# Performance work log

Measured on AMD Instinct MI355X. Metric: run time of the kernel, lower is better.

Reference implementation:

```python
import jax, jax.numpy as jnp
import numpy as np

N_NODES = 100000
N_EDGES = 1600000
D_IN = 128
D_H = 128
D_OUT = 64


def _glorot(key, shape):
    fan_in, fan_out = shape[0], shape[1]
    lim = np.sqrt(6.0 / (fan_in + fan_out)).astype(np.float32)
    return jax.random.uniform(key, shape, jnp.float32, -lim, lim)


def setup_inputs() -> dict:
    key = jax.random.key(0)
    ks = jax.random.split(key, 12)
    x = jax.random.normal(ks[0], (N_NODES, D_IN), jnp.float32)
    edge_index = jax.random.randint(ks[1], (2, N_EDGES), 0, N_NODES, jnp.int64)
    return {
        'x': x,
        'edge_index': edge_index,
        'Wl0': _glorot(ks[2], (D_IN, D_H)),  'bl0': jnp.zeros((D_H,), jnp.float32), 'Wr0': _glorot(ks[3], (D_IN, D_H)),
        'Wl1': _glorot(ks[4], (D_H, D_H)),   'bl1': jnp.zeros((D_H,), jnp.float32), 'Wr1': _glorot(ks[5], (D_H, D_H)),
        'Wl2': _glorot(ks[6], (D_H, D_H)),   'bl2': jnp.zeros((D_H,), jnp.float32), 'Wr2': _glorot(ks[7], (D_H, D_H)),
        'W':   _glorot(ks[8], (D_H, D_OUT)), 'b':   jnp.zeros((D_OUT,), jnp.float32),
    }


def _sage_conv(x, src, dst, inv_deg, Wl, bl, Wr):
    # mean aggregation of neighbor features at dst, then lin_l(agg) + lin_r(x)
    agg = jax.ops.segment_sum(x[src], dst, num_segments=N_NODES)  # [N, d]
    mean = agg * inv_deg  # [N, d]
    return mean @ Wl + bl + x @ Wr


def reference(x, edge_index, Wl0, bl0, Wr0, Wl1, bl1, Wr1, Wl2, bl2, Wr2, W, b):
    src, dst = edge_index[0], edge_index[1]
    deg = jax.ops.segment_sum(jnp.ones((N_EDGES,), jnp.float32), dst, num_segments=N_NODES)
    inv_deg = (1.0 / jnp.maximum(deg, 1.0))[:, None]  # [N, 1]
    h = jax.nn.relu(_sage_conv(x, src, dst, inv_deg, Wl0, bl0, Wr0))
    h = jax.nn.relu(_sage_conv(h, src, dst, inv_deg, Wl1, bl1, Wr1))
    h = jax.nn.relu(_sage_conv(h, src, dst, inv_deg, Wl2, bl2, Wr2))
    return h @ W + b
```

## Files before the change

### kernel.cpp

```cpp
#include <hip/hip_runtime.h>
#include <cstddef>

#define N_NODES 100000
#define N_EDGES 1600000
#define D 128
#define NB 782
#define CAP 3072
#define NBLK 1000
#define CHUNK 1600
#define OROW 784
#define WTOT (6 * 16384 + 8192)

typedef unsigned int u32;
typedef unsigned long long u64;
typedef float f32x4 __attribute__((ext_vector_type(4)));
typedef _Float16 f16x8 __attribute__((ext_vector_type(8)));

__device__ inline f16x8 mk16(u64 a, u64 b) {
  union { u64 q[2]; f16x8 v; } u;
  u.q[0] = a; u.q[1] = b;
  return u.v;
}

__device__ inline void acc8(float* a, uint2 d, float c) {
  a[0] += (float)(d.x & 0xFFu) * c;
  a[1] += (float)((d.x >> 8) & 0xFFu) * c;
  a[2] += (float)((d.x >> 16) & 0xFFu) * c;
  a[3] += (float)(d.x >> 24) * c;
  a[4] += (float)(d.y & 0xFFu) * c;
  a[5] += (float)((d.y >> 8) & 0xFFu) * c;
  a[6] += (float)((d.y >> 16) & 0xFFu) * c;
  a[7] += (float)(d.y >> 24) * c;
}

__device__ inline u64 dq4(u32 w, float c, float n) {
  float f0 = fmaf((float)(w & 0xFFu), c, n);
  float f1 = fmaf((float)((w >> 8) & 0xFFu), c, n);
  float f2 = fmaf((float)((w >> 16) & 0xFFu), c, n);
  float f3 = fmaf((float)(w >> 24), c, n);
  auto lo = __builtin_amdgcn_cvt_pkrtz(f0, f1);
  auto hi = __builtin_amdgcn_cvt_pkrtz(f2, f3);
  return (u64)__builtin_bit_cast(u32, lo) | ((u64)__builtin_bit_cast(u32, hi) << 32);
}


__global__ __launch_bounds__(256) void k_prep(
    const float* __restrict__ x,
    unsigned char* __restrict__ x8, float* __restrict__ sx,
    const float* __restrict__ w0, const float* __restrict__ w1, const float* __restrict__ w2,
    const float* __restrict__ w3, const float* __restrict__ w4, const float* __restrict__ w5,
    const float* __restrict__ w6, unsigned short* __restrict__ wt16) {
  int bid = blockIdx.x;
  int tid = threadIdx.x;
  if (bid < 6250) {
    int row = bid * 16 + (tid >> 4);
    int sub = tid & 15;
    const float* xr = x + (size_t)row * D + sub * 8;
    float4 v0 = *(const float4*)xr;
    float4 v1 = *(const float4*)(xr + 4);
    float vs[8] = {v0.x, v0.y, v0.z, v0.w, v1.x, v1.y, v1.z, v1.w};
    float m = 0.f;
#pragma unroll
    for (int j = 0; j < 8; j++) m = fmaxf(m, fabsf(vs[j]));
#pragma unroll
    for (int off = 1; off < 16; off <<= 1) m = fmaxf(m, __shfl_xor(m, off));
    m = fmaxf(m, 1e-8f);
    float inv = 127.0f / m;
    u64 pk = 0;
#pragma unroll
    for (int j = 0; j < 8; j++) {
      int qi = (int)rintf(vs[j] * inv) + 128;
      pk |= (u64)(u32)(qi & 255) << (8 * j);
    }
    *(u64*)(x8 + (size_t)row * D + sub * 8) = pk;
    if (sub == 0) sx[row] = m / 127.0f;
    return;
  }
  int i = (bid - 6250) * 256 + tid;
  if (i >= WTOT) return;
  float v;
  if (i < 6 * 16384) {
    int m = i >> 14;
    int j = i & 16383;
    int c = j >> 7, k = j & 127;
    const float* w = (m == 0) ? w0 : (m == 1) ? w1 : (m == 2) ? w2
                   : (m == 3) ? w3 : (m == 4) ? w4 : w5;
    v = w[k * 128 + c];
  } else {
    int j = i - 6 * 16384;
    int c = j >> 7, k = j & 127;
    v = w6[k * 64 + c];
  }
  _Float16 h = (_Float16)v;
  wt16[i] = __builtin_bit_cast(unsigned short, h);
}


__global__ __launch_bounds__(256) void k_scatter(const int* __restrict__ src,
                                                 const int* __restrict__ dst,
                                                 u32* __restrict__ binned,
                                                 u32* __restrict__ offs) {
  __shared__ int cnt[NB];
  __shared__ int lbase[NB + 1];
  __shared__ int wsum[256];
  __shared__ u32 stage[CHUNK];
  const int tid = threadIdx.x;
  for (int i = tid; i < NB; i += 256) cnt[i] = 0;
  __syncthreads();
  const int e0 = blockIdx.x * CHUNK;
  for (int e = e0 + tid; e < e0 + CHUNK; e += 256)
    atomicAdd(&cnt[dst[e] >> 7], 1);
  __syncthreads();
  int c[4], s = 0;
#pragma unroll
  for (int j = 0; j < 4; j++) {
    int i = tid * 4 + j;
    c[j] = (i < NB) ? cnt[i] : 0;
    s += c[j];
  }
  wsum[tid] = s;
  __syncthreads();
  for (int off = 1; off < 256; off <<= 1) {
    int t = (tid >= off) ? wsum[tid - off] : 0;
    __syncthreads();
    wsum[tid] += t;
    __syncthreads();
  }
  int run = wsum[tid] - s;
#pragma unroll
  for (int j = 0; j < 4; j++) {
    int i = tid * 4 + j;
    if (i < NB) { lbase[i] = run; run += c[j]; }
  }
  if (tid == 0) lbase[NB] = CHUNK;
  __syncthreads();
  for (int i = tid; i < NB; i += 256) cnt[i] = 0;
  __syncthreads();
  for (int e = e0 + tid; e < e0 + CHUNK; e += 256) {
    int d = dst[e];
    int bkt = d >> 7;
    int l = atomicAdd(&cnt[bkt], 1);
    stage[lbase[bkt] + l] = ((u32)(d & 127) << 17) | (u32)src[e];
  }
  u32* orow = offs + (size_t)blockIdx.x * OROW;
  for (int i = tid; i <= NB; i += 256) orow[i] = (u32)lbase[i];
  __syncthreads();
  u32* bseg = binned + (size_t)blockIdx.x * CHUNK;
  for (int i = tid; i < CHUNK / 4; i += 256)
    *(uint4*)(bseg + i * 4) = *(const uint4*)(stage + i * 4);
}


__global__ __launch_bounds__(256) void k_build(const u32* __restrict__ binned,
                                               const u32* __restrict__ offs,
                                               int* __restrict__ row_start,
                                               int* __restrict__ row_end,
                                               float* __restrict__ inv_deg,
                                               int* __restrict__ csr_src) {
  __shared__ u32 stage[CAP];
  __shared__ int deg[128], sc[128], cur[128];
  __shared__ int fill;
  const int b = blockIdx.x;
  const int tid = threadIdx.x;
  if (tid == 0) fill = 0;
  if (tid < 128) deg[tid] = 0;
  __syncthreads();
  for (int k = tid; k < NBLK; k += 256) {
    const u32* orow = offs + (size_t)k * OROW;
    int o0 = (int)orow[b], o1 = (int)orow[b + 1];
    int n = o1 - o0;
    if (n > 0) {
      int p = atomicAdd(&fill, n);
      const u32* q = binned + (size_t)k * CHUNK + o0;
      for (int j = 0; j < n; ++j) stage[p + j] = q[j];
    }
  }
  __syncthreads();
  const int total = fill;
  for (int e = tid; e < total; e += 256)
    atomicAdd(&deg[stage[e] >> 17], 1);
  __syncthreads();
  int dv = (tid < 128) ? deg[tid] : 0;
  if (tid < 128) sc[tid] = dv;
  __syncthreads();
  for (int off = 1; off < 128; off <<= 1) {
    int t = (tid >= off && tid < 128) ? sc[tid - off] : 0;
    __syncthreads();
    if (tid < 128) sc[tid] += t;
    __syncthreads();
  }
  const int cbase = b * CAP;
  if (tid < 128) {
    int excl = sc[tid] - dv;
    cur[tid] = excl;
    int node = (b << 7) + tid;
    if (node < N_NODES) {
      row_start[node] = cbase + excl;
      row_end[node] = cbase + excl + dv;
      inv_deg[node] = 1.0f / fmaxf((float)dv, 1.0f);
    }
  }
  __syncthreads();
  for (int e = tid; e < total; e += 256) {
    u32 w = stage[e];
    int dl = w >> 17;
    int pos = cbase + atomicAdd(&cur[dl], 1);
    csr_src[pos] = (int)(w & 0x1FFFFu);
  }
}


template <bool BIN, bool BOUT>
__global__ __launch_bounds__(256) void k_agg(const unsigned char* __restrict__ q8,
                                             const float* __restrict__ qs,
                                             const int* __restrict__ row_start,
                                             const int* __restrict__ row_end,
                                             const float* __restrict__ inv_deg,
                                             const int* __restrict__ csr_src,
                                             unsigned char* __restrict__ out8,
                                             float* __restrict__ sout) {
  int node = blockIdx.x * 16 + (threadIdx.x >> 4);
  if (node >= N_NODES) return;
  int sub = threadIdx.x & 15;
  int p0 = row_start[node], p1 = row_end[node];
  float a[8];
#pragma unroll
  for (int j = 0; j < 8; j++) a[j] = 0.f;
  float ssum = 0.f;
  int p = p0;
  for (; p + 8 <= p1; p += 8) {
    int s0 = csr_src[p], s1 = csr_src[p + 1], s2 = csr_src[p + 2], s3 = csr_src[p + 3];
    int s4 = csr_src[p + 4], s5 = csr_src[p + 5], s6 = csr_src[p + 6], s7 = csr_src[p + 7];
    uint2 d0 = *(const uint2*)(q8 + (size_t)s0 * D + sub * 8);
    uint2 d1 = *(const uint2*)(q8 + (size_t)s1 * D + sub * 8);
    uint2 d2 = *(const uint2*)(q8 + (size_t)s2 * D + sub * 8);
    uint2 d3 = *(const uint2*)(q8 + (size_t)s3 * D + sub * 8);
    uint2 d4 = *(const uint2*)(q8 + (size_t)s4 * D + sub * 8);
    uint2 d5 = *(const uint2*)(q8 + (size_t)s5 * D + sub * 8);
    uint2 d6 = *(const uint2*)(q8 + (size_t)s6 * D + sub * 8);
    uint2 d7 = *(const uint2*)(q8 + (size_t)s7 * D + sub * 8);
    float c0 = qs[s0], c1 = qs[s1], c2 = qs[s2], c3 = qs[s3];
    float c4 = qs[s4], c5 = qs[s5], c6 = qs[s6], c7 = qs[s7];
    acc8(a, d0, c0); acc8(a, d1, c1); acc8(a, d2, c2); acc8(a, d3, c3);
    acc8(a, d4, c4); acc8(a, d5, c5); acc8(a, d6, c6); acc8(a, d7, c7);
    if (BIN) ssum += ((c0 + c1) + (c2 + c3)) + ((c4 + c5) + (c6 + c7));
  }
  for (; p + 2 <= p1; p += 2) {
    int s0 = csr_src[p], s1 = csr_src[p + 1];
    uint2 d0 = *(const uint2*)(q8 + (size_t)s0 * D + sub * 8);
    uint2 d1 = *(const uint2*)(q8 + (size_t)s1 * D + sub * 8);
    float c0 = qs[s0], c1 = qs[s1];
    acc8(a, d0, c0); acc8(a, d1, c1);
    if (BIN) ssum += c0 + c1;
  }
  if (p < p1) {
    int s0 = csr_src[p];
    uint2 d0 = *(const uint2*)(q8 + (size_t)s0 * D + sub * 8);
    float c0 = qs[s0];
    acc8(a, d0, c0);
    if (BIN) ssum += c0;
  }
  float scl = inv_deg[node];
  float v[8];
#pragma unroll
  for (int j = 0; j < 8; j++) {
    float t = a[j];
    if (BIN) t -= 128.0f * ssum;
    v[j] = t * scl;
  }
  float m = 0.f;
#pragma unroll
  for (int j = 0; j < 8; j++) m = fmaxf(m, BOUT ? fabsf(v[j]) : v[j]);
#pragma unroll
  for (int off = 1; off < 16; off <<= 1) m = fmaxf(m, __shfl_xor(m, off));
  m = fmaxf(m, 1e-8f);
  u64 pk = 0;
  if (BOUT) {
    float inv = 127.0f / m;
#pragma unroll
    for (int j = 0; j < 8; j++) {
      int qi = (int)rintf(v[j] * inv) + 128;
      pk |= (u64)(u32)(qi & 255) << (8 * j);
    }
  } else {
    float inv = 255.0f / m;
#pragma unroll
    for (int j = 0; j < 8; j++) {
      u32 qi = (u32)(v[j] * inv + 0.5f);
      pk |= (u64)(qi & 255) << (8 * j);
    }
  }
  *(u64*)(out8 + (size_t)node * D + sub * 8) = pk;
  if (sub == 0) sout[node] = m / (BOUT ? 127.0f : 255.0f);
}


template <bool B0, bool B1>
__global__ __launch_bounds__(256) void k_gemm(
    const unsigned char* __restrict__ in0, const float* __restrict__ s0,
    const unsigned char* __restrict__ in1, const float* __restrict__ s1,
    const unsigned short* __restrict__ wt, const float* __restrict__ bias,
    unsigned char* __restrict__ h8out, float* __restrict__ shout) {
  __shared__ u64 sI[128][9];
  __shared__ u64 sW[128][9];
  __shared__ u32 rmaxb[128];
  __shared__ unsigned char h8t[128 * 144];

  const int tid = threadIdx.x;
  const int row0 = blockIdx.x * 128;
  const int lane = tid & 63;
  const int w = tid >> 6;
  const int wr = w >> 1, wc = w & 1;
  const int lrow = lane & 15, kb = lane >> 4;
  const int sr = tid >> 2, sq = tid & 3;

  f32x4 acc[4][4];
#pragma unroll
  for (int i = 0; i < 4; i++)
#pragma unroll
    for (int j = 0; j < 4; j++) acc[i][j] = (f32x4){0.f, 0.f, 0.f, 0.f};

  uint2 rd[2]; float rc[2];
  u64 rW[2][2];

  auto loadA = [&](int ch) {
    const unsigned char* inP = (ch >= 4) ? in1 : in0;
    const float* sP = (ch >= 4) ? s1 : s0;
    const int kc = (ch & 3) * 32;
#pragma unroll
    for (int it = 0; it < 2; ++it) {
      int g = row0 + sr + it * 64;
      uint2 d = make_uint2(0, 0);
      float c = 0.f;
      if (g < N_NODES) {
        d = *(const uint2*)(inP + (size_t)g * D + kc + sq * 8);
        c = sP[g];
      }
      rd[it] = d; rc[it] = c;
    }
  };
  auto loadW = [&](int ch) {
    const int s = ch >> 2;
    const int kc = (ch & 3) * 32;
    const unsigned short* wP = wt + (size_t)s * 16384;
#pragma unroll
    for (int it = 0; it < 2; ++it) {
      int c = sr + it * 64;
      const u64* pp = (const u64*)(wP + (size_t)c * D + kc + sq * 8);
      rW[it][0] = pp[0]; rW[it][1] = pp[1];
    }
  };

  loadA(0); loadW(0);
#pragma unroll
  for (int ch = 0; ch < 8; ++ch) {
    const bool biased = (ch < 4) ? B0 : B1;
    __syncthreads();
#pragma unroll
    for (int it = 0; it < 2; ++it) {
      int r = sr + it * 64;
      float c = rc[it];
      float n = biased ? -128.0f * c : 0.0f;
      sI[r][sq * 2] = dq4(rd[it].x, c, n);
      sI[r][sq * 2 + 1] = dq4(rd[it].y, c, n);
      sW[r][sq * 2] = rW[it][0]; sW[r][sq * 2 + 1] = rW[it][1];
    }
    __syncthreads();
    if (ch < 7) { loadA(ch + 1); loadW(ch + 1); }

    f16x8 fA[4], fB[4];
#pragma unroll
    for (int rt = 0; rt < 4; ++rt) {
      int rr = wr * 64 + rt * 16 + lrow;
      fA[rt] = mk16(sI[rr][kb * 2], sI[rr][kb * 2 + 1]);
    }
#pragma unroll
    for (int ct = 0; ct < 4; ++ct) {
      int cc = wc * 64 + ct * 16 + lrow;
      fB[ct] = mk16(sW[cc][kb * 2], sW[cc][kb * 2 + 1]);
    }
#pragma unroll
    for (int ct = 0; ct < 4; ++ct)
#pragma unroll
      for (int rt = 0; rt < 4; ++rt)
        acc[rt][ct] = __builtin_amdgcn_mfma_f32_16x16x32_f16(fA[rt], fB[ct], acc[rt][ct], 0, 0, 0);
  }

  if (tid < 128) rmaxb[tid] = 0;
  float bv[4];
#pragma unroll
  for (int ct = 0; ct < 4; ++ct) bv[ct] = bias[wc * 64 + ct * 16 + lrow];
#pragma unroll
  for (int ct = 0; ct < 4; ++ct)
#pragma unroll
    for (int rt = 0; rt < 4; ++rt)
#pragma unroll
      for (int r = 0; r < 4; ++r)
        acc[rt][ct][r] = fmaxf(acc[rt][ct][r] + bv[ct], 0.f);
  __syncthreads();
#pragma unroll
  for (int rt = 0; rt < 4; ++rt) {
#pragma unroll
    for (int r = 0; r < 4; ++r) {
      float m = fmaxf(fmaxf(acc[rt][0][r], acc[rt][1][r]),
                      fmaxf(acc[rt][2][r], acc[rt][3][r]));
      m = fmaxf(m, __shfl_xor(m, 1));
      m = fmaxf(m, __shfl_xor(m, 2));
      m = fmaxf(m, __shfl_xor(m, 4));
      m = fmaxf(m, __shfl_xor(m, 8));
      if (lrow == 0)
        atomicMax(&rmaxb[wr * 64 + rt * 16 + kb * 4 + r], __float_as_uint(m));
    }
  }
  __syncthreads();
#pragma unroll
  for (int rt = 0; rt < 4; ++rt) {
#pragma unroll
    for (int r = 0; r < 4; ++r) {
      int row = wr * 64 + rt * 16 + kb * 4 + r;
      float rm = fmaxf(__uint_as_float(rmaxb[row]), 1e-8f);
      float inv = 255.0f / rm;
#pragma unroll
      for (int ct = 0; ct < 4; ++ct) {
        u32 q = (u32)(acc[rt][ct][r] * inv + 0.5f);
        h8t[row * 144 + wc * 64 + ct * 16 + lrow] = (unsigned char)q;
      }
    }
  }
  __syncthreads();
  for (int idx = tid; idx < 128 * 8; idx += 256) {
    int row = idx >> 3, qq = idx & 7;
    int g = row0 + row;
    if (g < N_NODES)
      *(uint4*)(h8out + (size_t)g * D + qq * 16) =
          *(const uint4*)(h8t + row * 144 + qq * 16);
  }
  if (tid < 128 && row0 + tid < N_NODES)
    shout[row0 + tid] = fmaxf(__uint_as_float(rmaxb[tid]), 1e-8f) / 255.0f;
}


template <bool B0, bool B1>
__global__ __launch_bounds__(256) void k_gemm2(
    const unsigned char* __restrict__ in0, const float* __restrict__ s0,
    const unsigned char* __restrict__ in1, const float* __restrict__ s1,
    const unsigned short* __restrict__ wt, const float* __restrict__ bias,
    const unsigned short* __restrict__ w2, const float* __restrict__ b2,
    float* __restrict__ outp) {
  __shared__ __align__(16) char smem[128 * 33 * 8 + 2 * 128 * 9 * 8];
  u64 (*sH3)[33] = (u64(*)[33])smem;
  u64 (*sI)[9] = (u64(*)[9])(smem + 128 * 33 * 8);
  u64 (*sW)[9] = (u64(*)[9])(smem + 128 * 33 * 8 + 128 * 9 * 8);
  u64 (*sW2)[33] = (u64(*)[33])(smem + 128 * 33 * 8);

  const int tid = threadIdx.x;
  const int row0 = blockIdx.x * 128;
  const int lane = tid & 63;
  const int w = tid >> 6;
  const int wr = w >> 1, wc = w & 1;
  const int lrow = lane & 15, kb = lane >> 4;
  const int sr = tid >> 2, sq = tid & 3;

  f32x4 acc[4][4];
#pragma unroll
  for (int i = 0; i < 4; i++)
#pragma unroll
    for (int j = 0; j < 4; j++) acc[i][j] = (f32x4){0.f, 0.f, 0.f, 0.f};

  uint2 rd[2]; float rc[2];
  u64 rW[2][2];

  auto loadA = [&](int ch) {
    const unsigned char* inP = (ch >= 4) ? in1 : in0;
    const float* sP = (ch >= 4) ? s1 : s0;
    const int kc = (ch & 3) * 32;
#pragma unroll
    for (int it = 0; it < 2; ++it) {
      int g = row0 + sr + it * 64;
      uint2 d = make_uint2(0, 0);
      float c = 0.f;
      if (g < N_NODES) {
        d = *(const uint2*)(inP + (size_t)g * D + kc + sq * 8);
        c = sP[g];
      }
      rd[it] = d; rc[it] = c;
    }
  };
  auto loadW = [&](int ch) {
    const int s = ch >> 2;
    const int kc = (ch & 3) * 32;
    const unsigned short* wP = wt + (size_t)s * 16384;
#pragma unroll
    for (int it = 0; it < 2; ++it) {
      int c = sr + it * 64;
      const u64* pp = (const u64*)(wP + (size_t)c * D + kc + sq * 8);
      rW[it][0] = pp[0]; rW[it][1] = pp[1];
    }
  };

  loadA(0); loadW(0);
#pragma unroll
  for (int ch = 0; ch < 8; ++ch) {
    const bool biased = (ch < 4) ? B0 : B1;
    __syncthreads();
#pragma unroll
    for (int it = 0; it < 2; ++it) {
      int r = sr + it * 64;
      float c = rc[it];
      float n = biased ? -128.0f * c : 0.0f;
      sI[r][sq * 2] = dq4(rd[it].x, c, n);
      sI[r][sq * 2 + 1] = dq4(rd[it].y, c, n);
      sW[r][sq * 2] = rW[it][0]; sW[r][sq * 2 + 1] = rW[it][1];
    }
    __syncthreads();
    if (ch < 7) { loadA(ch + 1); loadW(ch + 1); }

    f16x8 fA[4], fB[4];
#pragma unroll
    for (int rt = 0; rt < 4; ++rt) {
      int rr = wr * 64 + rt * 16 + lrow;
      fA[rt] = mk16(sI[rr][kb * 2], sI[rr][kb * 2 + 1]);
    }
#pragma unroll
    for (int ct = 0; ct < 4; ++ct) {
      int cc = wc * 64 + ct * 16 + lrow;
      fB[ct] = mk16(sW[cc][kb * 2], sW[cc][kb * 2 + 1]);
    }
#pragma unroll
    for (int ct = 0; ct < 4; ++ct)
#pragma unroll
      for (int rt = 0; rt < 4; ++rt)
        acc[rt][ct] = __builtin_amdgcn_mfma_f32_16x16x32_f16(fA[rt], fB[ct], acc[rt][ct], 0, 0, 0);
  }

#pragma unroll
  for (int ct = 0; ct < 4; ++ct) {
    int col = wc * 64 + ct * 16 + lrow;
    float bv = bias[col];
#pragma unroll
    for (int rt = 0; rt < 4; ++rt) {
      int rbase = wr * 64 + rt * 16 + kb * 4;
#pragma unroll
      for (int r = 0; r < 4; ++r) {
        float v = fmaxf(acc[rt][ct][r] + bv, 0.f);
        _Float16 hv = (_Float16)v;
        ((unsigned short*)(&sH3[rbase + r][0]))[col] = __builtin_bit_cast(unsigned short, hv);
      }
    }
  }
  __syncthreads();
  for (int idx = tid; idx < 64 * 32; idx += 256) {
    int c = idx >> 5, j = idx & 31;
    sW2[c][j] = ((const u64*)(w2 + (size_t)c * D))[j];
  }
  __syncthreads();

  f32x4 acc2[4][2];
#pragma unroll
  for (int i = 0; i < 4; i++)
#pragma unroll
    for (int j = 0; j < 2; j++) acc2[i][j] = (f32x4){0.f, 0.f, 0.f, 0.f};

#pragma unroll
  for (int kc2 = 0; kc2 < 4; ++kc2) {
    f16x8 fA[4], fB[2];
#pragma unroll
    for (int rt = 0; rt < 4; ++rt) {
      int rr = wr * 64 + rt * 16 + lrow;
      fA[rt] = mk16(sH3[rr][kc2 * 8 + kb * 2], sH3[rr][kc2 * 8 + kb * 2 + 1]);
    }
#pragma unroll
    for (int ct = 0; ct < 2; ++ct) {
      int cc = wc * 32 + ct * 16 + lrow;
      fB[ct] = mk16(sW2[cc][kc2 * 8 + kb * 2], sW2[cc][kc2 * 8 + kb * 2 + 1]);
    }
#pragma unroll
    for (int ct = 0; ct < 2; ++ct)
#pragma unroll
      for (int rt = 0; rt < 4; ++rt)
        acc2[rt][ct] =
            __builtin_amdgcn_mfma_f32_16x16x32_f16(fA[rt], fB[ct], acc2[rt][ct], 0, 0, 0);
  }

#pragma unroll
  for (int ct = 0; ct < 2; ++ct) {
    int col = wc * 32 + ct * 16 + lrow;
    float bv = b2[col];
#pragma unroll
    for (int rt = 0; rt < 4; ++rt) {
#pragma unroll
      for (int r = 0; r < 4; ++r) {
        int g = row0 + wr * 64 + rt * 16 + kb * 4 + r;
        if (g < N_NODES) outp[(size_t)g * 64 + col] = acc2[rt][ct][r] + bv;
      }
    }
  }
}


extern "C" void kernel_launch(void* const* d_in, const int* in_sizes, int n_in,
                              void* d_out, int out_size, void* d_ws, size_t ws_size,
                              hipStream_t stream) {
  const float* x = (const float*)d_in[0];
  const int* edge = (const int*)d_in[1];
  const int* src = edge;
  const int* dst = edge + N_EDGES;
  const float* Wl0 = (const float*)d_in[2];
  const float* bl0 = (const float*)d_in[3];
  const float* Wr0 = (const float*)d_in[4];
  const float* Wl1 = (const float*)d_in[5];
  const float* bl1 = (const float*)d_in[6];
  const float* Wr1 = (const float*)d_in[7];
  const float* Wl2 = (const float*)d_in[8];
  const float* bl2 = (const float*)d_in[9];
  const float* Wr2 = (const float*)d_in[10];
  const float* W = (const float*)d_in[11];
  const float* b = (const float*)d_in[12];
  float* out = (float*)d_out;
  (void)ws_size; (void)n_in; (void)in_sizes; (void)out_size;

  char* ws = (char*)d_ws;
  float* sx = (float*)(ws);
  float* sh = (float*)(ws + (512ll << 10));
  float* sa = (float*)(ws + (1ll << 20));
  int* row_start = (int*)(ws + (2ll << 20));
  int* row_end = (int*)(ws + (3ll << 20));
  float* inv_deg = (float*)(ws + (4ll << 20));
  int* csr_src = (int*)(ws + (5ll << 20));
  u32* offs = (u32*)(ws + (15ll << 20));
  unsigned short* wt16 = (unsigned short*)(ws + (19ll << 20));
  unsigned char* agg8 = (unsigned char*)(ws + (20ll << 20));
  unsigned char* x8 = (unsigned char*)(ws + (33ll << 20));
  unsigned char* h8 = (unsigned char*)(ws + (46ll << 20));
  u32* binned = (u32*)(ws + (59ll << 20));

  k_prep<<<6250 + (WTOT + 255) / 256, 256, 0, stream>>>(
      x, x8, sx, Wl0, Wr0, Wl1, Wr1, Wl2, Wr2, W, wt16);
  k_scatter<<<NBLK, 256, 0, stream>>>(src, dst, binned, offs);
  k_build<<<NB, 256, 0, stream>>>(binned, offs, row_start, row_end, inv_deg, csr_src);

  const int agg_grid = (N_NODES + 15) / 16;
  const int gemm_grid = (N_NODES + 127) / 128;

  k_agg<true, true><<<agg_grid, 256, 0, stream>>>(
      x8, sx, row_start, row_end, inv_deg, csr_src, agg8, sa);
  k_gemm<true, true><<<gemm_grid, 256, 0, stream>>>(
      agg8, sa, x8, sx, wt16 + 0, bl0, h8, sh);
  k_agg<false, false><<<agg_grid, 256, 0, stream>>>(
      h8, sh, row_start, row_end, inv_deg, csr_src, agg8, sa);
  k_gemm<false, false><<<gemm_grid, 256, 0, stream>>>(
      agg8, sa, h8, sh, wt16 + 32768, bl1, h8, sh);
  k_agg<false, false><<<agg_grid, 256, 0, stream>>>(
      h8, sh, row_start, row_end, inv_deg, csr_src, agg8, sa);
  k_gemm2<false, false><<<gemm_grid, 256, 0, stream>>>(
      agg8, sa, h8, sh, wt16 + 65536, bl2, wt16 + 98304, b, out);
}
```

Baseline: 250.6 us.

## Merge edge scatter into prep kernel and widen aggregation gathers to 16 bytes

The edge-binning scatter is folded into the prep kernel as an extra range of blocks, removing one kernel launch and letting binning run alongside x quantization and weight conversion. The aggregation kernel now uses 8 lanes per node, each gathering 16 bytes per neighbor instead of 8. Neighbor indices and scales are loaded cooperatively once per group of eight edges and broadcast with shuffles. This cuts redundant index and scale loads and the number of gather instructions, at the cost of more registers per thread and a larger shared-memory footprint for all prep blocks.

Measured after the change: 263.8 us. +5.2%, slower.

```diff
diff --git a/kernel.cpp b/kernel.cpp
--- a/kernel.cpp
+++ b/kernel.cpp
@@ -10,6 +10,8 @@
 #define CHUNK 1600
 #define OROW 784
 #define WTOT (6 * 16384 + 8192)
+#define XBLK 6250
+#define WBLK ((WTOT + 255) / 256)
 
 typedef unsigned int u32;
 typedef unsigned long long u64;
@@ -22,15 +24,15 @@
   return u.v;
 }
 
-__device__ inline void acc8(float* a, uint2 d, float c) {
-  a[0] += (float)(d.x & 0xFFu) * c;
-  a[1] += (float)((d.x >> 8) & 0xFFu) * c;
-  a[2] += (float)((d.x >> 16) & 0xFFu) * c;
-  a[3] += (float)(d.x >> 24) * c;
-  a[4] += (float)(d.y & 0xFFu) * c;
-  a[5] += (float)((d.y >> 8) & 0xFFu) * c;
-  a[6] += (float)((d.y >> 16) & 0xFFu) * c;
-  a[7] += (float)(d.y >> 24) * c;
+__device__ inline void acc8(float* a, u32 dx, u32 dy, float c) {
+  a[0] += (float)(dx & 0xFFu) * c;
+  a[1] += (float)((dx >> 8) & 0xFFu) * c;
+  a[2] += (float)((dx >> 16) & 0xFFu) * c;
+  a[3] += (float)(dx >> 24) * c;
+  a[4] += (float)(dy & 0xFFu) * c;
+  a[5] += (float)((dy >> 8) & 0xFFu) * c;
+  a[6] += (float)((dy >> 16) & 0xFFu) * c;
+  a[7] += (float)(dy >> 24) * c;
 }
 
 __device__ inline u64 dq4(u32 w, float c, float n) {
@@ -49,11 +51,64 @@
     unsigned char* __restrict__ x8, float* __restrict__ sx,
     const float* __restrict__ w0, const float* __restrict__ w1, const float* __restrict__ w2,
     const float* __restrict__ w3, const float* __restrict__ w4, const float* __restrict__ w5,
-    const float* __restrict__ w6, unsigned short* __restrict__ wt16) {
-  int bid = blockIdx.x;
-  int tid = threadIdx.x;
-  if (bid < 6250) {
-    int row = bid * 16 + (tid >> 4);
+    const float* __restrict__ w6, unsigned short* __restrict__ wt16,
+    const int* __restrict__ src, const int* __restrict__ dst,
+    u32* __restrict__ binned, u32* __restrict__ offs) {
+  __shared__ int cnt[NB];
+  __shared__ int lbase[NB + 1];
+  __shared__ int wsum[256];
+  __shared__ u32 stage[CHUNK];
+  const int bid = blockIdx.x;
+  const int tid = threadIdx.x;
+
+  if (bid < NBLK) {
+    for (int i = tid; i < NB; i += 256) cnt[i] = 0;
+    __syncthreads();
+    const int e0 = bid * CHUNK;
+    for (int e = e0 + tid; e < e0 + CHUNK; e += 256)
+      atomicAdd(&cnt[dst[e] >> 7], 1);
+    __syncthreads();
+    int c[4], s = 0;
+#pragma unroll
+    for (int j = 0; j < 4; j++) {
+      int i = tid * 4 + j;
+      c[j] = (i < NB) ? cnt[i] : 0;
+      s += c[j];
+    }
+    wsum[tid] = s;
+    __syncthreads();
+    for (int off = 1; off < 256; off <<= 1) {
+      int t = (tid >= off) ? wsum[tid - off] : 0;
+      __syncthreads();
+      wsum[tid] += t;
+      __syncthreads();
+    }
+    int run = wsum[tid] - s;
+#pragma unroll
+    for (int j = 0; j < 4; j++) {
+      int i = tid * 4 + j;
+      if (i < NB) { lbase[i] = run; run += c[j]; }
+    }
+    if (tid == 0) lbase[NB] = CHUNK;
+    __syncthreads();
+    for (int i = tid; i < NB; i += 256) cnt[i] = 0;
+    __syncthreads();
+    for (int e = e0 + tid; e < e0 + CHUNK; e += 256) {
+      int d = dst[e];
+      int bkt = d >> 7;
+      int l = atomicAdd(&cnt[bkt], 1);
+      stage[lbase[bkt] + l] = ((u32)(d & 127) << 17) | (u32)src[e];
+    }
+    u32* orow = offs + (size_t)bid * OROW;
+    for (int i = tid; i <= NB; i += 256) orow[i] = (u32)lbase[i];
+    __syncthreads();
+    u32* bseg = binned + (size_t)bid * CHUNK;
+    for (int i = tid; i < CHUNK / 4; i += 256)
+      *(uint4*)(bseg + i * 4) = *(const uint4*)(stage + i * 4);
+    return;
+  }
+  if (bid < NBLK + XBLK) {
+    int row = (bid - NBLK) * 16 + (tid >> 4);
     int sub = tid & 15;
     const float* xr = x + (size_t)row * D + sub * 8;
     float4 v0 = *(const float4*)xr;
@@ -76,7 +131,7 @@
     if (sub == 0) sx[row] = m / 127.0f;
     return;
   }
-  int i = (bid - 6250) * 256 + tid;
+  int i = (bid - NBLK - XBLK) * 256 + tid;
   if (i >= WTOT) return;
   float v;
   if (i < 6 * 16384) {
@@ -96,61 +151,6 @@
 }
 
 
-__global__ __launch_bounds__(256) void k_scatter(const int* __restrict__ src,
-                                                 const int* __restrict__ dst,
-                                                 u32* __restrict__ binned,
-                                                 u32* __restrict__ offs) {
-  __shared__ int cnt[NB];
-  __shared__ int lbase[NB + 1];
-  __shared__ int wsum[256];
-  __shared__ u32 stage[CHUNK];
-  const int tid = threadIdx.x;
-  for (int i = tid; i < NB; i += 256) cnt[i] = 0;
-  __syncthreads();
-  const int e0 = blockIdx.x * CHUNK;
-  for (int e = e0 + tid; e < e0 + CHUNK; e += 256)
-    atomicAdd(&cnt[dst[e] >> 7], 1);
-  __syncthreads();
-  int c[4], s = 0;
-#pragma unroll
-  for (int j = 0; j < 4; j++) {
-    int i = tid * 4 + j;
-    c[j] = (i < NB) ? cnt[i] : 0;
-    s += c[j];
-  }
-  wsum[tid] = s;
-  __syncthreads();
-  for (int off = 1; off < 256; off <<= 1) {
-    int t = (tid >= off) ? wsum[tid - off] : 0;
-    __syncthreads();
-    wsum[tid] += t;
-    __syncthreads();
-  }
-  int run = wsum[tid] - s;
-#pragma unroll
-  for (int j = 0; j < 4; j++) {
-    int i = tid * 4 + j;
-    if (i < NB) { lbase[i] = run; run += c[j]; }
-  }
-  if (tid == 0) lbase[NB] = CHUNK;
-  __syncthreads();
-  for (int i = tid; i < NB; i += 256) cnt[i] = 0;
-  __syncthreads();
-  for (int e = e0 + tid; e < e0 + CHUNK; e += 256) {
-    int d = dst[e];
-    int bkt = d >> 7;
-    int l = atomicAdd(&cnt[bkt], 1);
-    stage[lbase[bkt] + l] = ((u32)(d & 127) << 17) | (u32)src[e];
-  }
-  u32* orow = offs + (size_t)blockIdx.x * OROW;
-  for (int i = tid; i <= NB; i += 256) orow[i] = (u32)lbase[i];
-  __syncthreads();
-  u32* bseg = binned + (size_t)blockIdx.x * CHUNK;
-  for (int i = tid; i < CHUNK / 4; i += 256)
-    *(uint4*)(bseg + i * 4) = *(const uint4*)(stage + i * 4);
-}
-
-
 __global__ __launch_bounds__(256) void k_build(const u32* __restrict__ binned,
                                                const u32* __restrict__ offs,
                                                int* __restrict__ row_start,
@@ -219,78 +219,73 @@
                                              const int* __restrict__ csr_src,
                                              unsigned char* __restrict__ out8,
                                              float* __restrict__ sout) {
-  int node = blockIdx.x * 16 + (threadIdx.x >> 4);
+  int node = blockIdx.x * 32 + (threadIdx.x >> 3);
   if (node >= N_NODES) return;
-  int sub = threadIdx.x & 15;
+  int sub = threadIdx.x & 7;
   int p0 = row_start[node], p1 = row_end[node];
-  float a[8];
-#pragma unroll
-  for (int j = 0; j < 8; j++) a[j] = 0.f;
+  float a[16];
+#pragma unroll
+  for (int j = 0; j < 16; j++) a[j] = 0.f;
   float ssum = 0.f;
   int p = p0;
   for (; p + 8 <= p1; p += 8) {
-    int s0 = csr_src[p], s1 = csr_src[p + 1], s2 = csr_src[p + 2], s3 = csr_src[p + 3];
-    int s4 = csr_src[p + 4], s5 = csr_src[p + 5], s6 = csr_src[p + 6], s7 = csr_src[p + 7];
-    uint2 d0 = *(const uint2*)(q8 + (size_t)s0 * D + sub * 8);
-    uint2 d1 = *(const uint2*)(q8 + (size_t)s1 * D + sub * 8);
-    uint2 d2 = *(const uint2*)(q8 + (size_t)s2 * D + sub * 8);
-    uint2 d3 = *(const uint2*)(q8 + (size_t)s3 * D + sub * 8);
-    uint2 d4 = *(const uint2*)(q8 + (size_t)s4 * D + sub * 8);
-    uint2 d5 = *(const uint2*)(q8 + (size_t)s5 * D + sub * 8);
-    uint2 d6 = *(const uint2*)(q8 + (size_t)s6 * D + sub * 8);
-    uint2 d7 = *(const uint2*)(q8 + (size_t)s7 * D + sub * 8);
-    float c0 = qs[s0], c1 = qs[s1], c2 = qs[s2], c3 = qs[s3];
-    float c4 = qs[s4], c5 = qs[s5], c6 = qs[s6], c7 = qs[s7];
-    acc8(a, d0, c0); acc8(a, d1, c1); acc8(a, d2, c2); acc8(a, d3, c3);
-    acc8(a, d4, c4); acc8(a, d5, c5); acc8(a, d6, c6); acc8(a, d7, c7);
-    if (BIN) ssum += ((c0 + c1) + (c2 + c3)) + ((c4 + c5) + (c6 + c7));
-  }
-  for (; p + 2 <= p1; p += 2) {
-    int s0 = csr_src[p], s1 = csr_src[p + 1];
-    uint2 d0 = *(const uint2*)(q8 + (size_t)s0 * D + sub * 8);
-    uint2 d1 = *(const uint2*)(q8 + (size_t)s1 * D + sub * 8);
-    float c0 = qs[s0], c1 = qs[s1];
-    acc8(a, d0, c0); acc8(a, d1, c1);
-    if (BIN) ssum += c0 + c1;
-  }
-  if (p < p1) {
-    int s0 = csr_src[p];
-    uint2 d0 = *(const uint2*)(q8 + (size_t)s0 * D + sub * 8);
-    float c0 = qs[s0];
-    acc8(a, d0, c0);
-    if (BIN) ssum += c0;
+    int myidx = csr_src[p + sub];
+    float myc = qs[myidx];
+#pragma unroll
+    for (int j = 0; j < 8; j++) {
+      int s = __shfl(myidx, j, 8);
+      float c = __shfl(myc, j, 8);
+      uint4 d = *(const uint4*)(q8 + (size_t)s * D + sub * 16);
+      acc8(a, d.x, d.y, c);
+      acc8(a + 8, d.z, d.w, c);
+      if (BIN) ssum += c;
+    }
+  }
+  for (; p < p1; ++p) {
+    int s = csr_src[p];
+    float c = qs[s];
+    uint4 d = *(const uint4*)(q8 + (size_t)s * D + sub * 16);
+    acc8(a, d.x, d.y, c);
+    acc8(a + 8, d.z, d.w, c);
+    if (BIN) ssum += c;
   }
   float scl = inv_deg[node];
-  float v[8];
-#pragma unroll
-  for (int j = 0; j < 8; j++) {
+  float v[16];
+#pragma unroll
+  for (int j = 0; j < 16; j++) {
     float t = a[j];
     if (BIN) t -= 128.0f * ssum;
     v[j] = t * scl;
   }
   float m = 0.f;
 #pragma unroll
-  for (int j = 0; j < 8; j++) m = fmaxf(m, BOUT ? fabsf(v[j]) : v[j]);
-#pragma unroll
-  for (int off = 1; off < 16; off <<= 1) m = fmaxf(m, __shfl_xor(m, off));
+  for (int j = 0; j < 16; j++) m = fmaxf(m, BOUT ? fabsf(v[j]) : v[j]);
+#pragma unroll
+  for (int off = 1; off < 8; off <<= 1) m = fmaxf(m, __shfl_xor(m, off));
   m = fmaxf(m, 1e-8f);
-  u64 pk = 0;
+  u64 pk0 = 0, pk1 = 0;
   if (BOUT) {
     float inv = 127.0f / m;
 #pragma unroll
     for (int j = 0; j < 8; j++) {
-      int qi = (int)rintf(v[j] * inv) + 128;
-      pk |= (u64)(u32)(qi & 255) << (8 * j);
+      int q0 = (int)rintf(v[j] * inv) + 128;
+      int q1 = (int)rintf(v[j + 8] * inv) + 128;
+      pk0 |= (u64)(u32)(q0 & 255) << (8 * j);
+      pk1 |= (u64)(u32)(q1 & 255) << (8 * j);
     }
   } else {
     float inv = 255.0f / m;
 #pragma unroll
     for (int j = 0; j < 8; j++) {
-      u32 qi = (u32)(v[j] * inv + 0.5f);
-      pk |= (u64)(qi & 255) << (8 * j);
-    }
-  }
-  *(u64*)(out8 + (size_t)node * D + sub * 8) = pk;
+      u32 q0 = (u32)(v[j] * inv + 0.5f);
+      u32 q1 = (u32)(v[j + 8] * inv + 0.5f);
+      pk0 |= (u64)(q0 & 255) << (8 * j);
+      pk1 |= (u64)(q1 & 255) << (8 * j);
+    }
+  }
+  union { u64 q[2]; uint4 u; } st;
+  st.q[0] = pk0; st.q[1] = pk1;
+  *(uint4*)(out8 + (size_t)node * D + sub * 16) = st.u;
   if (sub == 0) sout[node] = m / (BOUT ? 127.0f : 255.0f);
 }
 
@@ -634,12 +629,11 @@
   unsigned char* h8 = (unsigned char*)(ws + (46ll << 20));
   u32* binned = (u32*)(ws + (59ll << 20));
 
-  k_prep<<<6250 + (WTOT + 255) / 256, 256, 0, stream>>>(
-      x, x8, sx, Wl0, Wr0, Wl1, Wr1, Wl2, Wr2, W, wt16);
-  k_scatter<<<NBLK, 256, 0, stream>>>(src, dst, binned, offs);
+  k_prep<<<NBLK + XBLK + WBLK, 256, 0, stream>>>(
+      x, x8, sx, Wl0, Wr0, Wl1, Wr1, Wl2, Wr2, W, wt16, src, dst, binned, offs);
   k_build<<<NB, 256, 0, stream>>>(binned, offs, row_start, row_end, inv_deg, csr_src);
 
-  const int agg_grid = (N_NODES + 15) / 16;
+  const int agg_grid = (N_NODES + 31) / 32;
   const int gemm_grid = (N_NODES + 127) / 128;
 
   k_agg<true, true><<<agg_grid, 256, 0, stream>>>(
```
